# Optimization experiments

Hardware: AMD Instinct MI355X
Metric: run time of the kernel (lower is better)

Reference implementation:

```python
import jax, jax.numpy as jnp
import numpy as np

CONF_THRESH = 0.25
IOU_THRESH = 0.45
MAX_DET = 300          # max_per_img
MIN_DET = 1            # min_per_img
PRE_NMS_TOPK = 512     # fixed candidate pool per image (jit-friendly stand-in for conf filtering)
MAX_WH = 7680.0        # class-offset trick for class-aware NMS (as in yolov5)
ANCHORS_PER_CELL = 3   # matches `ids // 3` in the wrapper


def setup_inputs() -> dict:
    key = jax.random.key(0)
    k1, k2, k3, k4 = jax.random.split(key, 4)
    bs, n, nc = 64, 25200, 3
    cxcy = jax.random.uniform(k1, (bs, n, 2), dtype=jnp.float32) * 640.0
    wh = jax.random.uniform(k2, (bs, n, 2), dtype=jnp.float32) * 64.0 + 2.0
    obj = jax.random.uniform(k3, (bs, n, 1), dtype=jnp.float32)
    cls = jax.random.uniform(k4, (bs, n, nc), dtype=jnp.float32)
    pred = jnp.concatenate([cxcy, wh, obj, cls], axis=-1)  # [bs, n, 5+nc]
    return {"pred": pred}


def reference(pred):
    """Confidence scoring + class-aware greedy NMS (yolov5-style), fixed-shape outputs."""
    bs = pred.shape[0]
    K = PRE_NMS_TOPK
    obj = pred[..., 4]                                   # [bs, n]
    cls_scores = obj[..., None] * pred[..., 5:]          # conf = obj * cls (multi_label=False)
    best = jnp.max(cls_scores, axis=-1)                  # [bs, n]
    cls_id = jnp.argmax(cls_scores, axis=-1)             # [bs, n]

    # pre-NMS candidate selection (sorted by score desc)
    topv, topi = jax.lax.top_k(best, K)                  # [bs, K]
    xywh = jnp.take_along_axis(pred[..., :4], topi[..., None], axis=1)
    boxes = jnp.concatenate([xywh[..., :2] - xywh[..., 2:] * 0.5,
                             xywh[..., :2] + xywh[..., 2:] * 0.5], axis=-1)  # xyxy
    cid = jnp.take_along_axis(cls_id, topi, axis=1)
    conf_ok = topv > CONF_THRESH

    # class offset so boxes of different classes never overlap
    ob = boxes + (cid.astype(boxes.dtype) * MAX_WH)[..., None]

    # pairwise IoU per image: [bs, K, K]
    area = (ob[..., 2] - ob[..., 0]) * (ob[..., 3] - ob[..., 1])
    lt = jnp.maximum(ob[:, :, None, :2], ob[:, None, :, :2])
    rb = jnp.minimum(ob[:, :, None, 2:], ob[:, None, :, 2:])
    whi = jnp.clip(rb - lt, 0.0)
    inter = whi[..., 0] * whi[..., 1]
    iou = inter / (area[:, :, None] + area[:, None, :] - inter + 1e-7)

    upper = jnp.arange(K)[None, :] > jnp.arange(K)[:, None]  # j > i (candidates sorted by score)

    def body(i, suppressed):
        keep_i = jnp.logical_not(suppressed[:, i])           # [bs]
        new_sup = keep_i[:, None] & (iou[:, i, :] > IOU_THRESH) & upper[i]
        return suppressed | new_sup

    suppressed = jax.lax.fori_loop(0, K, body, jnp.zeros((bs, K), dtype=bool))
    keep = jnp.logical_not(suppressed)

    # enforce min_per_img: the first MIN_DET kept boxes survive even below conf_thresh
    rank = jnp.cumsum(keep.astype(jnp.int32), axis=1)
    valid = keep & (conf_ok | (rank <= MIN_DET))

    # pack top MAX_DET surviving detections (padded, fixed shape)
    sel = jnp.where(valid, topv, -1.0)
    sv, si = jax.lax.top_k(sel, MAX_DET)                  # [bs, MAX_DET]
    out_valid = sv > -0.5
    out_boxes = jnp.take_along_axis(boxes, si[..., None], axis=1)
    out_scores = jnp.take_along_axis(topv, si, axis=1)
    out_cls = jnp.take_along_axis(cid, si, axis=1)
    out_ids = jnp.take_along_axis(topi, si, axis=1) // ANCHORS_PER_CELL  # matches `ids // 3`
    out_boxes = jnp.where(out_valid[..., None], out_boxes, 0.0)
    out_scores = jnp.where(out_valid, out_scores, 0.0)
    return out_boxes, out_scores, out_cls, out_ids, out_valid
```

## Files before the change

### kernel.cpp

```cpp
#include <hip/hip_runtime.h>
#include <cstdint>
#include <cstddef>

#define BS      64
#define NPRED   25200
#define KTOP    512
#define MAXDET  300
#define NBINS   4096
#define CAP     1024
#define NTHR    1024
#define CONF_T  0.25f
#define IOU_T   0.45f
#define MAXWH   7680.0f

__global__ __launch_bounds__(NTHR) void yolo_k(const float* __restrict__ pred,
                                               float* __restrict__ out) {
  __shared__ __align__(16) unsigned char smem[121280];
  __shared__ float sv[CAP];
  __shared__ int   si[CAP];
  __shared__ unsigned int supW[16];
  __shared__ int cutoff_s, cnt_s;

  float*        scoreL = (float*)smem;
  unsigned int* hist   = (unsigned int*)(smem + 100800);
  unsigned int* gsum   = (unsigned int*)(smem + 117184);
  float* bx0 = (float*)(smem);
  float* bx1 = (float*)(smem + 2048);
  float* bx2 = (float*)(smem + 4096);
  float* bx3 = (float*)(smem + 6144);
  float* ox0 = (float*)(smem + 8192);
  float* oy0 = (float*)(smem + 10240);
  float* ox1 = (float*)(smem + 12288);
  float* oy1 = (float*)(smem + 14336);
  float* areaL = (float*)(smem + 16384);
  int*   cidL  = (int*)(smem + 18432);
  unsigned int* mask = (unsigned int*)(smem + 20480);
  int*   scanb = (int*)(smem + 55296);

  const int tid = threadIdx.x;
  const int img = blockIdx.x;
  const float* __restrict__ base = pred + (size_t)img * (NPRED * 8);

  for (int b = tid; b < NBINS; b += NTHR) hist[b] = 0u;
  if (tid == 0) cnt_s = 0;
  __syncthreads();
  for (int e = tid; e < NPRED; e += NTHR) {
    const float4 q = *reinterpret_cast<const float4*>(base + (size_t)e * 8 + 4);
    float m = fmaxf(q.x * q.y, fmaxf(q.x * q.z, q.x * q.w));
    scoreL[e] = m;
    int b = (int)(m * (float)NBINS);
    b = min(max(b, 0), NBINS - 1);
    atomicAdd(&hist[b], 1u);
  }
  __syncthreads();
  gsum[tid] = hist[4 * tid] + hist[4 * tid + 1] + hist[4 * tid + 2] + hist[4 * tid + 3];
  __syncthreads();
  for (int d = 1; d < NTHR; d <<= 1) {
    unsigned v = gsum[tid] + ((tid + d < NTHR) ? gsum[tid + d] : 0u);
    __syncthreads();
    gsum[tid] = v;
    __syncthreads();
  }
  if (gsum[tid] >= KTOP && (tid == NTHR - 1 || gsum[tid + 1] < KTOP)) {
    unsigned acc = (tid == NTHR - 1) ? 0u : gsum[tid + 1];
    int b = 4 * tid + 4;
    do { --b; acc += hist[b]; } while (acc < KTOP && b > 4 * tid);
    cutoff_s = b;
  }
  __syncthreads();
  const int cutoff = cutoff_s;

  for (int e = tid; e < NPRED; e += NTHR) {
    float v = scoreL[e];
    int b = (int)(v * (float)NBINS);
    b = min(max(b, 0), NBINS - 1);
    if (b >= cutoff) {
      int p = atomicAdd(&cnt_s, 1);
      if (p < CAP) { sv[p] = v; si[p] = e; }
    }
  }
  __syncthreads();
  {
    int cnt = min(cnt_s, CAP);
    if (tid >= cnt) { sv[tid] = -1e30f; si[tid] = 0x7fffffff; }
  }
  __syncthreads();

  for (int k = 2; k <= CAP; k <<= 1) {
    for (int j = k >> 1; j > 0; j >>= 1) {
      int ixj = tid ^ j;
      if (ixj > tid) {
        float va = sv[tid], vb = sv[ixj];
        int ia = si[tid], ib = si[ixj];
        bool aWorse = (va < vb) || (va == vb && ia > ib);
        bool up = ((tid & k) == 0);
        if (up == aWorse) {
          sv[tid] = vb; sv[ixj] = va;
          si[tid] = ib; si[ixj] = ia;
        }
      }
      __syncthreads();
    }
  }

  if (tid < KTOP) {
    int gi = si[tid];
    const float4 a = *reinterpret_cast<const float4*>(base + (size_t)gi * 8);
    const float4 q = *reinterpret_cast<const float4*>(base + (size_t)gi * 8 + 4);
    float p0 = q.x * q.y, p1 = q.x * q.z, p2 = q.x * q.w;
    float m = fmaxf(p0, fmaxf(p1, p2));
    int c = (p0 == m) ? 0 : ((p1 == m) ? 1 : 2);
    float x0 = a.x - a.z * 0.5f;
    float y0 = a.y - a.w * 0.5f;
    float x1 = a.x + a.z * 0.5f;
    float y1 = a.y + a.w * 0.5f;
    float co = (float)c * MAXWH;
    bx0[tid] = x0; bx1[tid] = y0; bx2[tid] = x1; bx3[tid] = y1;
    float o0 = x0 + co, o1 = y0 + co, o2 = x1 + co, o3 = y1 + co;
    ox0[tid] = o0; oy0[tid] = o1; ox1[tid] = o2; oy1[tid] = o3;
    areaL[tid] = (o2 - o0) * (o3 - o1);
    cidL[tid] = c;
  }
  __syncthreads();

  for (int w = tid; w < KTOP * 16; w += NTHR) {
    int i = w & (KTOP - 1);
    int jw = w >> 9;
    unsigned m = 0u;
    int jbase = jw << 5;
    if (jbase + 31 > i) {
      float ax0 = ox0[i], ay0 = oy0[i], ax1 = ox1[i], ay1 = oy1[i];
      float aa = areaL[i];
#pragma unroll
      for (int bb = 0; bb < 32; ++bb) {
        int j = jbase + bb;
        if (j > i) {
          float ix0 = fmaxf(ax0, ox0[j]);
          float iy0 = fmaxf(ay0, oy0[j]);
          float ix1 = fminf(ax1, ox1[j]);
          float iy1 = fminf(ay1, oy1[j]);
          float iw = fmaxf(ix1 - ix0, 0.0f);
          float ih = fmaxf(iy1 - iy0, 0.0f);
          float inter = iw * ih;
          float denom = aa + areaL[j] - inter + 1e-7f;
          if (inter > IOU_T * denom) m |= (1u << bb);
        }
      }
    }
    mask[i * 17 + jw] = m;
  }
  __syncthreads();

  if (tid < 16) {
    unsigned s = 0u;
    const int lane = tid;
    for (int c = 0; c < KTOP / 16; ++c) {
      const int rb = c * 16;
      const int wi = rb >> 5;
      const int b0 = rb & 31;
      unsigned myrow[16], diag[16];
#pragma unroll
      for (int r = 0; r < 16; ++r) {
        myrow[r] = mask[(rb + r) * 17 + lane];
        diag[r]  = mask[(rb + r) * 17 + wi];
      }
      unsigned wcur = __shfl(s, wi, 64);
#pragma unroll
      for (int r = 0; r < 16; ++r) {
        if (!((wcur >> (b0 + r)) & 1u)) { s |= myrow[r]; wcur |= diag[r]; }
      }
    }
    supW[lane] = s;
  }
  __syncthreads();

  bool keep = false, valid = false;
  float score = 0.0f;
  if (tid < KTOP) {
    keep = !((supW[tid >> 5] >> (tid & 31)) & 1u);
    score = sv[tid];
    scanb[tid] = keep ? 1 : 0;
  }
  __syncthreads();
  for (int d = 1; d < KTOP; d <<= 1) {
    int v = 0;
    if (tid < KTOP) { v = scanb[tid]; if (tid >= d) v += scanb[tid - d]; }
    __syncthreads();
    if (tid < KTOP) scanb[tid] = v;
    __syncthreads();
  }
  if (tid < KTOP) {
    int rank = scanb[tid];
    valid = keep && ((score > CONF_T) || (rank <= 1));
  }
  __syncthreads();
  if (tid < KTOP) scanb[tid] = valid ? 1 : 0;
  __syncthreads();
  for (int d = 1; d < KTOP; d <<= 1) {
    int v = 0;
    if (tid < KTOP) { v = scanb[tid]; if (tid >= d) v += scanb[tid - d]; }
    __syncthreads();
    if (tid < KTOP) scanb[tid] = v;
    __syncthreads();
  }
  if (tid < KTOP) {
    int vs = scanb[tid];
    int nvalid = scanb[KTOP - 1];
    int pos = valid ? (vs - 1) : (nvalid + tid - vs);
    if (pos < MAXDET) {
      const int SB = BS * MAXDET;
      float* outBoxes  = out;
      float* outScores = out + (size_t)SB * 4;
      float* outCls    = outScores + SB;
      float* outIds    = outCls + SB;
      float* outValid  = outIds + SB;
      size_t row = (size_t)img * MAXDET + pos;
      if (valid) {
        outBoxes[row * 4 + 0] = bx0[tid];
        outBoxes[row * 4 + 1] = bx1[tid];
        outBoxes[row * 4 + 2] = bx2[tid];
        outBoxes[row * 4 + 3] = bx3[tid];
        outScores[row] = score;
      } else {
        outBoxes[row * 4 + 0] = 0.0f;
        outBoxes[row * 4 + 1] = 0.0f;
        outBoxes[row * 4 + 2] = 0.0f;
        outBoxes[row * 4 + 3] = 0.0f;
        outScores[row] = 0.0f;
      }
      outCls[row]   = (float)cidL[tid];
      outIds[row]   = (float)(si[tid] / 3);
      outValid[row] = valid ? 1.0f : 0.0f;
    }
  }
}

extern "C" void kernel_launch(void* const* d_in, const int* in_sizes, int n_in,
                              void* d_out, int out_size, void* d_ws, size_t ws_size,
                              hipStream_t stream) {
  (void)in_sizes; (void)n_in; (void)out_size; (void)d_ws; (void)ws_size;
  const float* pred = (const float*)d_in[0];
  float* out = (float*)d_out;
  yolo_k<<<BS, NTHR, 0, stream>>>(pred, out);
}
```

Measured before the change: 147.3 us.

## Split histogram into grid-wide kernel and use register/shuffle sort, ballot scans, ballot IoU masks

```diff
diff --git a/kernel.cpp b/kernel.cpp
--- a/kernel.cpp
+++ b/kernel.cpp
@@ -12,99 +12,151 @@
 #define CONF_T  0.25f
 #define IOU_T   0.45f
 #define MAXWH   7680.0f
-
-__global__ __launch_bounds__(NTHR) void yolo_k(const float* __restrict__ pred,
-                                               float* __restrict__ out) {
-  __shared__ __align__(16) unsigned char smem[121280];
-  __shared__ float sv[CAP];
-  __shared__ int   si[CAP];
+#define MSTRIDE 17
+
+__device__ __forceinline__ unsigned long long shflx64(unsigned long long v, int m) {
+  unsigned lo = __shfl_xor((unsigned)(v & 0xffffffffull), m, 64);
+  unsigned hi = __shfl_xor((unsigned)(v >> 32), m, 64);
+  return (((unsigned long long)hi) << 32) | lo;
+}
+
+__device__ __forceinline__ float scoreOf(const float4& q) {
+  return fmaxf(q.x * q.y, fmaxf(q.x * q.z, q.x * q.w));
+}
+
+__global__ __launch_bounds__(256) void score_hist_k(const float* __restrict__ pred,
+                                                    unsigned int* __restrict__ ghist) {
+  const int img = blockIdx.y;
+  const int e = blockIdx.x * 256 + threadIdx.x;
+  if (e >= NPRED) return;
+  const float4 q = *reinterpret_cast<const float4*>(pred + ((size_t)img * NPRED + e) * 8 + 4);
+  float m = scoreOf(q);
+  int b = (int)(m * (float)NBINS);
+  b = min(max(b, 0), NBINS - 1);
+  atomicAdd(&ghist[(img << 12) + b], 1u);
+}
+
+template<bool GHIST>
+__global__ __launch_bounds__(NTHR) void nms_k(const float* __restrict__ pred,
+                                              const unsigned int* __restrict__ ghist,
+                                              float* __restrict__ out) {
+  __shared__ unsigned long long keysL[CAP];
+  __shared__ __align__(16) unsigned int maskA[KTOP * MSTRIDE];
+  __shared__ float ox0[KTOP], oy0[KTOP], ox1[KTOP], oy1[KTOP], areaL[KTOP];
+  __shared__ float bx0[KTOP], bx1[KTOP], bx2[KTOP], bx3[KTOP];
+  __shared__ float svL[KTOP]; __shared__ int siL[KTOP]; __shared__ int cidL[KTOP];
   __shared__ unsigned int supW[16];
-  __shared__ int cutoff_s, cnt_s;
-
-  float*        scoreL = (float*)smem;
-  unsigned int* hist   = (unsigned int*)(smem + 100800);
-  unsigned int* gsum   = (unsigned int*)(smem + 117184);
-  float* bx0 = (float*)(smem);
-  float* bx1 = (float*)(smem + 2048);
-  float* bx2 = (float*)(smem + 4096);
-  float* bx3 = (float*)(smem + 6144);
-  float* ox0 = (float*)(smem + 8192);
-  float* oy0 = (float*)(smem + 10240);
-  float* ox1 = (float*)(smem + 12288);
-  float* oy1 = (float*)(smem + 14336);
-  float* areaL = (float*)(smem + 16384);
-  int*   cidL  = (int*)(smem + 18432);
-  unsigned int* mask = (unsigned int*)(smem + 20480);
-  int*   scanb = (int*)(smem + 55296);
+  __shared__ unsigned int wtot[16];
+  __shared__ int woff[8];
+  __shared__ int cutoff_s, cnt_s, nvalid_s;
 
   const int tid = threadIdx.x;
+  const int lane = tid & 63;
+  const int wid = tid >> 6;
   const int img = blockIdx.x;
   const float* __restrict__ base = pred + (size_t)img * (NPRED * 8);
 
-  for (int b = tid; b < NBINS; b += NTHR) hist[b] = 0u;
   if (tid == 0) cnt_s = 0;
-  __syncthreads();
+
+  unsigned h0, h1, h2, h3;
+  if (GHIST) {
+    const uint4 h = *reinterpret_cast<const uint4*>(ghist + ((size_t)img << 12) + (tid << 2));
+    h0 = h.x; h1 = h.y; h2 = h.z; h3 = h.w;
+  } else {
+    unsigned int* hist = maskA;
+    for (int b = tid; b < NBINS; b += NTHR) hist[b] = 0u;
+    __syncthreads();
+    for (int e = tid; e < NPRED; e += NTHR) {
+      const float4 q = *reinterpret_cast<const float4*>(base + (size_t)e * 8 + 4);
+      float m = scoreOf(q);
+      int b = (int)(m * (float)NBINS);
+      b = min(max(b, 0), NBINS - 1);
+      atomicAdd(&hist[b], 1u);
+    }
+    __syncthreads();
+    const uint4 h = *reinterpret_cast<const uint4*>(hist + (tid << 2));
+    h0 = h.x; h1 = h.y; h2 = h.z; h3 = h.w;
+  }
+
+  unsigned g = h0 + h1 + h2 + h3;
+  unsigned s = g;
+#pragma unroll
+  for (int d = 1; d < 64; d <<= 1) {
+    unsigned o = __shfl_down(s, d, 64);
+    if (lane + d < 64) s += o;
+  }
+  if (lane == 0) wtot[wid] = s;
+  __syncthreads();
+  if (tid < 16) {
+    unsigned t = wtot[tid];
+#pragma unroll
+    for (int d = 1; d < 16; d <<= 1) {
+      unsigned o = __shfl_down(t, d, 64);
+      if (tid + d < 16) t += o;
+    }
+    wtot[tid] = t;
+  }
+  __syncthreads();
+  unsigned S = s + ((wid < 15) ? wtot[wid + 1] : 0u);
+  if (S >= KTOP && (S - g) < KTOP) {
+    unsigned acc = S - g;
+    int cut;
+    acc += h3;
+    if (acc >= KTOP) cut = 4 * tid + 3;
+    else {
+      acc += h2;
+      if (acc >= KTOP) cut = 4 * tid + 2;
+      else {
+        acc += h1;
+        if (acc >= KTOP) cut = 4 * tid + 1;
+        else cut = 4 * tid;
+      }
+    }
+    cutoff_s = cut;
+  }
+  __syncthreads();
+  const int cutoff = cutoff_s;
+
   for (int e = tid; e < NPRED; e += NTHR) {
     const float4 q = *reinterpret_cast<const float4*>(base + (size_t)e * 8 + 4);
-    float m = fmaxf(q.x * q.y, fmaxf(q.x * q.z, q.x * q.w));
-    scoreL[e] = m;
+    float m = scoreOf(q);
     int b = (int)(m * (float)NBINS);
-    b = min(max(b, 0), NBINS - 1);
-    atomicAdd(&hist[b], 1u);
-  }
-  __syncthreads();
-  gsum[tid] = hist[4 * tid] + hist[4 * tid + 1] + hist[4 * tid + 2] + hist[4 * tid + 3];
-  __syncthreads();
-  for (int d = 1; d < NTHR; d <<= 1) {
-    unsigned v = gsum[tid] + ((tid + d < NTHR) ? gsum[tid + d] : 0u);
-    __syncthreads();
-    gsum[tid] = v;
-    __syncthreads();
-  }
-  if (gsum[tid] >= KTOP && (tid == NTHR - 1 || gsum[tid + 1] < KTOP)) {
-    unsigned acc = (tid == NTHR - 1) ? 0u : gsum[tid + 1];
-    int b = 4 * tid + 4;
-    do { --b; acc += hist[b]; } while (acc < KTOP && b > 4 * tid);
-    cutoff_s = b;
-  }
-  __syncthreads();
-  const int cutoff = cutoff_s;
-
-  for (int e = tid; e < NPRED; e += NTHR) {
-    float v = scoreL[e];
-    int b = (int)(v * (float)NBINS);
     b = min(max(b, 0), NBINS - 1);
     if (b >= cutoff) {
       int p = atomicAdd(&cnt_s, 1);
-      if (p < CAP) { sv[p] = v; si[p] = e; }
-    }
-  }
-  __syncthreads();
-  {
-    int cnt = min(cnt_s, CAP);
-    if (tid >= cnt) { sv[tid] = -1e30f; si[tid] = 0x7fffffff; }
-  }
-  __syncthreads();
+      if (p < CAP) {
+        keysL[p] = (((unsigned long long)__float_as_uint(m)) << 32)
+                 | (unsigned)(0x7FFFFFFF - e);
+      }
+    }
+  }
+  __syncthreads();
+  const int cnt = min(cnt_s, CAP);
+  unsigned long long key = (tid < cnt) ? keysL[tid] : 0ull;
 
   for (int k = 2; k <= CAP; k <<= 1) {
     for (int j = k >> 1; j > 0; j >>= 1) {
-      int ixj = tid ^ j;
-      if (ixj > tid) {
-        float va = sv[tid], vb = sv[ixj];
-        int ia = si[tid], ib = si[ixj];
-        bool aWorse = (va < vb) || (va == vb && ia > ib);
-        bool up = ((tid & k) == 0);
-        if (up == aWorse) {
-          sv[tid] = vb; sv[ixj] = va;
-          si[tid] = ib; si[ixj] = ia;
-        }
-      }
-      __syncthreads();
+      unsigned long long p;
+      if (j >= 64) {
+        __syncthreads();
+        keysL[tid] = key;
+        __syncthreads();
+        p = keysL[tid ^ j];
+      } else {
+        p = shflx64(key, j);
+      }
+      bool lower = ((tid & j) == 0);
+      bool descR = ((tid & k) == 0);
+      bool takeMax = (lower == descR);
+      bool pGreater = (p > key);
+      key = (takeMax == pGreater) ? p : key;
     }
   }
 
   if (tid < KTOP) {
-    int gi = si[tid];
+    int gi = 0x7FFFFFFF - (int)(unsigned)(key & 0xffffffffull);
+    if ((unsigned)gi >= NPRED) gi = 0;
+    float v = __uint_as_float((unsigned)(key >> 32));
     const float4 a = *reinterpret_cast<const float4*>(base + (size_t)gi * 8);
     const float4 q = *reinterpret_cast<const float4*>(base + (size_t)gi * 8 + 4);
     float p0 = q.x * q.y, p1 = q.x * q.z, p2 = q.x * q.w;
@@ -120,40 +172,47 @@
     ox0[tid] = o0; oy0[tid] = o1; ox1[tid] = o2; oy1[tid] = o3;
     areaL[tid] = (o2 - o0) * (o3 - o1);
     cidL[tid] = c;
-  }
-  __syncthreads();
-
-  for (int w = tid; w < KTOP * 16; w += NTHR) {
-    int i = w & (KTOP - 1);
-    int jw = w >> 9;
-    unsigned m = 0u;
-    int jbase = jw << 5;
-    if (jbase + 31 > i) {
-      float ax0 = ox0[i], ay0 = oy0[i], ax1 = ox1[i], ay1 = oy1[i];
-      float aa = areaL[i];
-#pragma unroll
-      for (int bb = 0; bb < 32; ++bb) {
-        int j = jbase + bb;
-        if (j > i) {
-          float ix0 = fmaxf(ax0, ox0[j]);
-          float iy0 = fmaxf(ay0, oy0[j]);
-          float ix1 = fminf(ax1, ox1[j]);
-          float iy1 = fminf(ay1, oy1[j]);
-          float iw = fmaxf(ix1 - ix0, 0.0f);
-          float ih = fmaxf(iy1 - iy0, 0.0f);
-          float inter = iw * ih;
-          float denom = aa + areaL[j] - inter + 1e-7f;
-          if (inter > IOU_T * denom) m |= (1u << bb);
-        }
-      }
-    }
-    mask[i * 17 + jw] = m;
+    svL[tid] = v; siL[tid] = gi;
+  }
+  for (int w = tid; w < KTOP * MSTRIDE; w += NTHR) maskA[w] = 0u;
+  __syncthreads();
+
+  {
+    const int jb = wid & 7;
+    const int half = wid >> 3;
+    const int j = (jb << 6) + lane;
+    const float jx0 = ox0[j], jy0 = oy0[j], jx1 = ox1[j], jy1 = oy1[j], ja = areaL[j];
+    const int iend = (jb << 6) + 63;
+    for (int ibase = 0; ibase < iend; ibase += 64) {
+      float cx0 = ox0[ibase + lane], cy0 = oy0[ibase + lane];
+      float cx1 = ox1[ibase + lane], cy1 = oy1[ibase + lane];
+      float ca = areaL[ibase + lane];
+      int bbend = min(64, iend - ibase);
+      for (int bb = half; bb < bbend; bb += 2) {
+        float ix0 = __shfl(cx0, bb, 64);
+        float iy0 = __shfl(cy0, bb, 64);
+        float ix1 = __shfl(cx1, bb, 64);
+        float iy1 = __shfl(cy1, bb, 64);
+        float ia  = __shfl(ca,  bb, 64);
+        int i = ibase + bb;
+        float xx0 = fmaxf(ix0, jx0);
+        float yy0 = fmaxf(iy0, jy0);
+        float xx1 = fminf(ix1, jx1);
+        float yy1 = fminf(iy1, jy1);
+        float iw = fmaxf(xx1 - xx0, 0.0f);
+        float ih = fmaxf(yy1 - yy0, 0.0f);
+        float inter = iw * ih;
+        float denom = ia + ja - inter + 1e-7f;
+        bool sup = (inter > IOU_T * denom) && (j > i);
+        unsigned long long b = __ballot(sup);
+        if (lane < 2) maskA[i * MSTRIDE + (jb << 1) + lane] = (unsigned)(b >> (lane << 5));
+      }
+    }
   }
   __syncthreads();
 
   if (tid < 16) {
-    unsigned s = 0u;
-    const int lane = tid;
+    unsigned sst = 0u;
     for (int c = 0; c < KTOP / 16; ++c) {
       const int rb = c * 16;
       const int wi = rb >> 5;
@@ -161,51 +220,53 @@
       unsigned myrow[16], diag[16];
 #pragma unroll
       for (int r = 0; r < 16; ++r) {
-        myrow[r] = mask[(rb + r) * 17 + lane];
-        diag[r]  = mask[(rb + r) * 17 + wi];
-      }
-      unsigned wcur = __shfl(s, wi, 64);
+        myrow[r] = maskA[(rb + r) * MSTRIDE + tid];
+        diag[r]  = maskA[(rb + r) * MSTRIDE + wi];
+      }
+      unsigned wcur = __shfl(sst, wi, 64);
 #pragma unroll
       for (int r = 0; r < 16; ++r) {
-        if (!((wcur >> (b0 + r)) & 1u)) { s |= myrow[r]; wcur |= diag[r]; }
-      }
-    }
-    supW[lane] = s;
-  }
-  __syncthreads();
-
-  bool keep = false, valid = false;
+        if (!((wcur >> (b0 + r)) & 1u)) { sst |= myrow[r]; wcur |= diag[r]; }
+      }
+    }
+    supW[tid] = sst;
+  }
+  __syncthreads();
+
+  bool keep = false;
   float score = 0.0f;
   if (tid < KTOP) {
     keep = !((supW[tid >> 5] >> (tid & 31)) & 1u);
-    score = sv[tid];
-    scanb[tid] = keep ? 1 : 0;
-  }
-  __syncthreads();
-  for (int d = 1; d < KTOP; d <<= 1) {
-    int v = 0;
-    if (tid < KTOP) { v = scanb[tid]; if (tid >= d) v += scanb[tid - d]; }
-    __syncthreads();
-    if (tid < KTOP) scanb[tid] = v;
-    __syncthreads();
-  }
+    score = svL[tid];
+  }
+  unsigned long long balK = __ballot(keep);
+  int wpre = __popcll(balK & ((1ull << lane) - 1ull));
+  if (lane == 63 && wid < 8) wtot[wid] = (unsigned)(wpre + (keep ? 1 : 0));
+  __syncthreads();
+  if (tid == 0) {
+    int a = 0;
+    for (int w = 0; w < 8; ++w) { woff[w] = a; a += (int)wtot[w]; }
+  }
+  __syncthreads();
+  bool valid = false;
   if (tid < KTOP) {
-    int rank = scanb[tid];
+    int rank = woff[wid] + wpre + (keep ? 1 : 0);
     valid = keep && ((score > CONF_T) || (rank <= 1));
   }
   __syncthreads();
-  if (tid < KTOP) scanb[tid] = valid ? 1 : 0;
-  __syncthreads();
-  for (int d = 1; d < KTOP; d <<= 1) {
-    int v = 0;
-    if (tid < KTOP) { v = scanb[tid]; if (tid >= d) v += scanb[tid - d]; }
-    __syncthreads();
-    if (tid < KTOP) scanb[tid] = v;
-    __syncthreads();
-  }
+  unsigned long long balV = __ballot(valid);
+  int vpre = __popcll(balV & ((1ull << lane) - 1ull));
+  if (lane == 63 && wid < 8) wtot[wid] = (unsigned)(vpre + (valid ? 1 : 0));
+  __syncthreads();
+  if (tid == 0) {
+    int a = 0;
+    for (int w = 0; w < 8; ++w) { woff[w] = a; a += (int)wtot[w]; }
+    nvalid_s = a;
+  }
+  __syncthreads();
   if (tid < KTOP) {
-    int vs = scanb[tid];
-    int nvalid = scanb[KTOP - 1];
+    int vs = woff[wid] + vpre + (valid ? 1 : 0);
+    int nvalid = nvalid_s;
     int pos = valid ? (vs - 1) : (nvalid + tid - vs);
     if (pos < MAXDET) {
       const int SB = BS * MAXDET;
@@ -229,7 +290,7 @@
         outScores[row] = 0.0f;
       }
       outCls[row]   = (float)cidL[tid];
-      outIds[row]   = (float)(si[tid] / 3);
+      outIds[row]   = (float)(siL[tid] / 3);
       outValid[row] = valid ? 1.0f : 0.0f;
     }
   }
@@ -238,8 +299,16 @@
 extern "C" void kernel_launch(void* const* d_in, const int* in_sizes, int n_in,
                               void* d_out, int out_size, void* d_ws, size_t ws_size,
                               hipStream_t stream) {
-  (void)in_sizes; (void)n_in; (void)out_size; (void)d_ws; (void)ws_size;
+  (void)in_sizes; (void)n_in; (void)out_size;
   const float* pred = (const float*)d_in[0];
   float* out = (float*)d_out;
-  yolo_k<<<BS, NTHR, 0, stream>>>(pred, out);
-}
+  const size_t need = (size_t)BS * NBINS * sizeof(unsigned int);
+  if (d_ws != nullptr && ws_size >= need) {
+    unsigned int* ghist = (unsigned int*)d_ws;
+    hipMemsetAsync(d_ws, 0, need, stream);
+    score_hist_k<<<dim3((NPRED + 255) / 256, BS), 256, 0, stream>>>(pred, ghist);
+    nms_k<true><<<BS, NTHR, 0, stream>>>(pred, ghist, out);
+  } else {
+    nms_k<false><<<BS, NTHR, 0, stream>>>(pred, nullptr, out);
+  }
+}
```

After: 241.2 us. +63.7%, slower.
